# Performance work log

Measured on AMD Instinct MI355X. Metric: run time of the kernel, lower is better.

## Reference

```python
import jax, jax.numpy as jnp
import numpy as np

N = 8192      # nodes
DIN = 128     # in_channels
DH = 64       # hidden_channels (dim_out, num_heads=1)
DOUT = 32     # out_channels
RATIO = 0.5
K_KEEP = int(np.ceil(RATIO * N))  # SAGPooling keep count (single graph)
LN_EPS = 1e-5


def _linear_params(k, fan_in, fan_out):
    kw, kb = jax.random.split(k)
    W = jax.random.normal(kw, (fan_in, fan_out), dtype=jnp.float32) / jnp.sqrt(jnp.float32(fan_in))
    b = jax.random.normal(kb, (fan_out,), dtype=jnp.float32) * 0.01
    return W, b


def setup_inputs() -> dict:
    key = jax.random.key(0)
    ks = jax.random.split(key, 8)
    x = jax.random.normal(ks[0], (N, DIN), dtype=jnp.float32)
    batch = jnp.zeros((N,), dtype=jnp.int64)  # single graph
    Wq, bq = _linear_params(ks[1], DIN, DH)
    Wk, bk = _linear_params(ks[2], DIN, DH)
    Wv, bv = _linear_params(ks[3], DIN, DH)
    gcn_W, gcn_b = _linear_params(ks[4], DH, DH)       # GCNConv weight/bias
    score_W, score_b = _linear_params(ks[5], DH, 1)    # SAGPooling score GCNConv
    ln_g = jnp.ones((DH,), dtype=jnp.float32)
    ln_b = jnp.zeros((DH,), dtype=jnp.float32)
    head_W, head_b = _linear_params(ks[6], DH, DOUT)
    return dict(x=x, batch=batch, Wq=Wq, bq=bq, Wk=Wk, bk=bk, Wv=Wv, bv=bv,
                gcn_W=gcn_W, gcn_b=gcn_b, score_W=score_W, score_b=score_b,
                ln_g=ln_g, ln_b=ln_b, head_W=head_W, head_b=head_b)


def _forward(x, Wq, bq, Wk, bk, Wv, bv, gcn_W, gcn_b, score_W, score_b,
             ln_g, ln_b, head_W, head_b):
    # --- self-attention over all nodes (num_heads = 1) ---
    Q = x @ Wq + bq                                        # [N, DH]
    K = x @ Wk + bk
    V = x @ Wv + bv
    attn = jax.nn.softmax(Q @ K.T / jnp.sqrt(jnp.float32(DH)), axis=-1)  # [N, N]
    h = attn @ V                                           # [N, DH]

    # --- edge construction: threshold attention, ensure self-loops ---
    # (attn > 0.5).nonzero() -> edge set; empty -> self-loop fallback; then
    # add_self_loops. Dense equivalent: A = max(mask, I).
    eye = jnp.eye(N, dtype=x.dtype)
    A = jnp.maximum((attn > 0.5).astype(x.dtype), eye)     # [N, N], diag = 1

    # symmetric GCN normalization  D^{-1/2} A D^{-1/2}
    dinv = jax.lax.rsqrt(A.sum(axis=1))                    # [N]
    An = dinv[:, None] * A * dinv[None, :]                 # [N, N]

    # --- GCNConv layer ---
    g = An @ (h @ gcn_W) + gcn_b                           # [N, DH]

    # --- SAGPooling: GCNConv scorer -> tanh -> global top-k (single graph) ---
    score = jnp.tanh((An @ (g @ score_W) + score_b).squeeze(-1))  # [N]
    top_scores, perm = jax.lax.top_k(score, K_KEEP)        # sorted desc, like PyG topk
    xp = g[perm] * top_scores[:, None]                     # [K, DH], multiplier = 1

    # --- LayerNorm + ReLU (dropout is identity in eval) ---
    mu = xp.mean(axis=-1, keepdims=True)
    var = xp.var(axis=-1, keepdims=True)
    xp = (xp - mu) * jax.lax.rsqrt(var + LN_EPS) * ln_g + ln_b
    xp = jax.nn.relu(xp)

    # --- prediction head ---
    return xp @ head_W + head_b                            # [K, DOUT]


def reference(x, batch, Wq, bq, Wk, bk, Wv, bv, gcn_W, gcn_b,
              score_W, score_b, ln_g, ln_b, head_W, head_b):
    del batch  # single graph; grouping has no effect on the math
    return _forward(x, Wq, bq, Wk, bk, Wv, bv, gcn_W, gcn_b,
                    score_W, score_b, ln_g, ln_b, head_W, head_b)
```

## Files before the change

kernel.cpp:

```cpp
#include <hip/hip_runtime.h>
#include <hip/hip_bf16.h>
#include <cstdio>

typedef __hip_bfloat16 bf16;
typedef __attribute__((ext_vector_type(8))) short v8s;
typedef __attribute__((ext_vector_type(4))) short v4s;
typedef __attribute__((ext_vector_type(4))) float v4f;
typedef __attribute__((ext_vector_type(4))) double v4d;

#define MFMA16(a, b, c) __builtin_amdgcn_mfma_f32_16x16x32_bf16((a), (b), (c), 0, 0, 0)

#define NN 8192
#define DIN 128
#define DH 64
#define DOUT 32
#define KKEEP 4096
#define SPLITS 8
#define SPATT 8

__device__ __forceinline__ float bf2f(bf16 v) { return __bfloat162float(v); }
__device__ __forceinline__ short f2bfs(float f) {
  __hip_bfloat16 h = __float2bfloat16(f);
  return *reinterpret_cast<short*>(&h);
}
__device__ __forceinline__ bf16 f2bf(float v) { return __float2bfloat16(v); }

__device__ __forceinline__ double exp_d(double s) {
  const double L2E    = 1.4426950408889634074;
  const double LN2_HI = 6.93147180369123816490e-01;
  const double LN2_LO = 1.90821492927058770002e-10;
  double t  = s * L2E;
  double kf = rint(t);
  double r  = fma(-kf, LN2_HI, s);
  r = fma(-kf, LN2_LO, r);
  double p = 1.0 / 362880.0;
  p = fma(p, r, 1.0 / 40320.0);
  p = fma(p, r, 1.0 / 5040.0);
  p = fma(p, r, 1.0 / 720.0);
  p = fma(p, r, 1.0 / 120.0);
  p = fma(p, r, 1.0 / 24.0);
  p = fma(p, r, 1.0 / 6.0);
  p = fma(p, r, 0.5);
  p = fma(p, r, 1.0);
  p = fma(p, r, 1.0);
  int k = (int)kf;
  long long bits = ((long long)(1023 + k)) << 52;
  double sc = __longlong_as_double(bits);
  return p * sc;
}

__global__ void k0_ucb(const float* __restrict__ gW, const float* __restrict__ sW,
                       const float* __restrict__ gb, double* __restrict__ u) {
  int c = threadIdx.x;
  double acc = 0.0, accb = 0.0;
  for (int d = 0; d < DH; ++d) {
    double swd = (double)sW[d];
    acc  = fma((double)gW[c * DH + d], swd, acc);
    accb = fma((double)gb[d], swd, accb);
  }
  u[c] = acc;
  if (c == 0) u[64] = accb;
}

__global__ __launch_bounds__(256) void k1_prep(
    const float* __restrict__ x, const float* __restrict__ Wq, const float* __restrict__ bq,
    const float* __restrict__ Wk, const float* __restrict__ bk, const float* __restrict__ Wv,
    const float* __restrict__ bv, const double* __restrict__ u,
    double* __restrict__ Qd, double* __restrict__ Kd, double* __restrict__ w,
    bf16* __restrict__ Qb, bf16* __restrict__ Kb, bf16* __restrict__ Vt) {
  __shared__ double xs[16][DIN];
  int t = threadIdx.x;
  int nb = blockIdx.x * 16;
  for (int idx = t; idx < 16 * DIN; idx += 256)
    xs[idx >> 7][idx & 127] = (double)x[(size_t)nb * DIN + idx];
  __syncthreads();
  int d = t & 63;
  int sub = t >> 6;
  double bqd = (double)bq[d];
  double bkd = (double)bk[d];
  double bvd = (double)bv[d];
  double ud = u[d];
  for (int pass = 0; pass < 4; ++pass) {
    int n = pass * 4 + sub;
    double aq = bqd, ak = bkd, av = bvd;
#pragma unroll 8
    for (int c = 0; c < DIN; ++c) {
      double xv = xs[n][c];
      aq = fma(xv, (double)Wq[c * DH + d], aq);
      ak = fma(xv, (double)Wk[c * DH + d], ak);
      av = fma(xv, (double)Wv[c * DH + d], av);
    }
    aq *= 0.125;
    int node = nb + n;
    Qd[(size_t)node * DH + d] = aq;
    Kd[(size_t)node * DH + d] = ak;
    Qb[(size_t)node * DH + d] = f2bf((float)aq);
    Kb[(size_t)node * DH + d] = f2bf((float)ak);
    Vt[(size_t)d * NN + node] = f2bf((float)av);
    double pw = av * ud;
#pragma unroll
    for (int off = 32; off; off >>= 1) pw += __shfl_xor(pw, off);
    if (d == 0) w[node] = pw;
  }
}

__global__ __launch_bounds__(256) void k2_scores(
    const double* __restrict__ Qd, const double* __restrict__ Kd, const double* __restrict__ w,
    double* __restrict__ Zp, double* __restrict__ Wp, double* __restrict__ Ep, int* __restrict__ Jp) {
  __shared__ __align__(16) double Kbuf[2][16][66];
  const int t = threadIdx.x;
  const int wv = t >> 6;
  const int l = t & 63;
  const int li = l & 15, lg = l >> 4;
  const int rb = (blockIdx.x & 127) * 64;
  const int sp = blockIdx.x >> 7;
  const int cbeg = sp * (NN / SPLITS);

  double qreg[16];
  const double* qrow = Qd + (size_t)(rb + 16 * wv + li) * DH + lg;
#pragma unroll
  for (int tt = 0; tt < 16; ++tt) qreg[tt] = qrow[4 * tt];

  {
    const double* src = Kd + (size_t)cbeg * DH;
    int r = t >> 4, c = (t & 15) * 4;
    *(double2*)&Kbuf[0][r][c]     = *(const double2*)&src[r * DH + c];
    *(double2*)&Kbuf[0][r][c + 2] = *(const double2*)&src[r * DH + c + 2];
  }
  __syncthreads();

  double Zt[4] = {0, 0, 0, 0}, Wt[4] = {0, 0, 0, 0}, Et[4] = {-1, -1, -1, -1};
  int Jt[4] = {0, 0, 0, 0};

  const int NT = (NN / SPLITS) / 16;
  for (int kt = 0; kt < NT; ++kt) {
    const int buf = kt & 1;
    if (kt + 1 < NT) {
      const double* src = Kd + (size_t)(cbeg + (kt + 1) * 16) * DH;
      int r = t >> 4, c = (t & 15) * 4;
      *(double2*)&Kbuf[buf ^ 1][r][c]     = *(const double2*)&src[r * DH + c];
      *(double2*)&Kbuf[buf ^ 1][r][c + 2] = *(const double2*)&src[r * DH + c + 2];
    }
    v4d acc = (v4d){0.0, 0.0, 0.0, 0.0};
#pragma unroll
    for (int tt = 0; tt < 16; ++tt) {
      double bfrag = Kbuf[buf][li][4 * tt + lg];
      acc = __builtin_amdgcn_mfma_f64_16x16x4f64(qreg[tt], bfrag, acc, 0, 0, 0);
    }
    const int col = cbeg + kt * 16 + li;
    const double wj = w[col];
#pragma unroll
    for (int v = 0; v < 4; ++v) {
      double e = exp_d(acc[v]);
      Zt[v] += e;
      Wt[v] = fma(e, wj, Wt[v]);
      if (e > Et[v]) { Et[v] = e; Jt[v] = col; }
    }
    __syncthreads();
  }

#pragma unroll
  for (int v = 0; v < 4; ++v) {
#pragma unroll
    for (int m = 1; m < 16; m <<= 1) {
      Zt[v] += __shfl_xor(Zt[v], m);
      Wt[v] += __shfl_xor(Wt[v], m);
      double e2 = __shfl_xor(Et[v], m);
      int j2 = __shfl_xor(Jt[v], m);
      if (e2 > Et[v] || (e2 == Et[v] && j2 < Jt[v])) { Et[v] = e2; Jt[v] = j2; }
    }
  }
  if (li == 0) {
#pragma unroll
    for (int v = 0; v < 4; ++v) {
      int row = rb + 16 * wv + lg + 4 * v;
      Zp[sp * NN + row] = Zt[v];
      Wp[sp * NN + row] = Wt[v];
      Ep[sp * NN + row] = Et[v];
      Jp[sp * NN + row] = Jt[v];
    }
  }
}

__global__ void k3_combine(const double* __restrict__ Zp, const double* __restrict__ Wp,
                           const double* __restrict__ Ep, const int* __restrict__ Jp,
                           double* __restrict__ tau, int* __restrict__ extra, int* __restrict__ jmA) {
  int i = blockIdx.x * 256 + threadIdx.x;
  double Z = 0, W = 0, E = -1;
  int J = 0;
  for (int sp = 0; sp < SPLITS; ++sp) {
    Z += Zp[sp * NN + i];
    W += Wp[sp * NN + i];
    double e = Ep[sp * NN + i];
    if (e > E || (e == E && Jp[sp * NN + i] < J)) { E = e; J = Jp[sp * NN + i]; }
  }
  tau[i] = W / Z;
  extra[i] = (E > 0.5 * Z) && (J != i);
  jmA[i] = J & (NN - 1);
}

__global__ __launch_bounds__(256) void k4_mfma(const bf16* __restrict__ Qb, const bf16* __restrict__ Kb,
                                               const bf16* __restrict__ Vt,
                                               float* __restrict__ hp, float* __restrict__ zp) {
  __shared__ __align__(16) short P[4][16 * 40];
  const int t = threadIdx.x;
  const int wv = t >> 6;
  const int l = t & 63, g = l >> 4, li = l & 15;
  const int qb = (blockIdx.x & 127) * 64 + wv * 16;
  const int sp = blockIdx.x >> 7;
  short* Pw = &P[wv][0];
  const v8s q0 = *(const v8s*)(Qb + (size_t)(qb + li) * DH + g * 8);
  const v8s q1 = *(const v8s*)(Qb + (size_t)(qb + li) * DH + 32 + g * 8);
  v4f hacc[4];
#pragma unroll
  for (int db = 0; db < 4; ++db) hacc[db] = (v4f){0.f, 0.f, 0.f, 0.f};
  float zl = 0.f;
  const int kbeg = sp * (NN / SPATT);
  for (int jb = kbeg; jb < kbeg + NN / SPATT; jb += 32) {
    const bf16* kp = Kb + (size_t)(jb + li) * DH + g * 8;
    v8s ka0 = *(const v8s*)(kp);
    v8s ka1 = *(const v8s*)(kp + 32);
    v8s kb0 = *(const v8s*)(kp + 16 * DH);
    v8s kb1 = *(const v8s*)(kp + 16 * DH + 32);
    v4f c0 = (v4f){0.f, 0.f, 0.f, 0.f}, c1 = (v4f){0.f, 0.f, 0.f, 0.f};
    c0 = MFMA16(ka0, q0, c0);
    c0 = MFMA16(ka1, q1, c0);
    c1 = MFMA16(kb0, q0, c1);
    c1 = MFMA16(kb1, q1, c1);
    v4s p0, p1;
#pragma unroll
    for (int r = 0; r < 4; ++r) {
      short b0 = f2bfs(__expf(c0[r]));
      short b1 = f2bfs(__expf(c1[r]));
      p0[r] = b0;
      p1[r] = b1;
      zl += bf2f(*reinterpret_cast<bf16*>(&b0));
      zl += bf2f(*reinterpret_cast<bf16*>(&b1));
    }
    *(v4s*)&Pw[li * 40 + g * 4] = p0;
    *(v4s*)&Pw[li * 40 + 16 + g * 4] = p1;
    __syncthreads();
    v8s pf = *(const v8s*)&Pw[li * 40 + g * 8];
#pragma unroll
    for (int db = 0; db < 4; ++db) {
      const v8s vb = *(const v8s*)(Vt + (size_t)(db * 16 + li) * NN + jb + g * 8);
      hacc[db] = MFMA16(pf, vb, hacc[db]);
    }
    __syncthreads();
  }
  zl += __shfl_xor(zl, 16);
  zl += __shfl_xor(zl, 32);
  if (g == 0) zp[sp * NN + qb + li] = zl;
#pragma unroll
  for (int r = 0; r < 4; ++r) {
    int row = qb + g * 4 + r;
#pragma unroll
    for (int db = 0; db < 4; ++db)
      hp[((size_t)sp * NN + row) * DH + db * 16 + li] = hacc[db][r];
  }
}

__global__ __launch_bounds__(256) void k4_comb(const float* __restrict__ hp, const float* __restrict__ zp,
                                               float* __restrict__ h) {
  int i = blockIdx.x * 256 + threadIdx.x;
  int row = i >> 6;
  float Z = 0.f, H = 0.f;
#pragma unroll
  for (int sp = 0; sp < SPATT; ++sp) {
    Z += zp[sp * NN + row];
    H += hp[(size_t)sp * NN * DH + i];
  }
  h[i] = H / Z;
}

__global__ void k5_t(const double* __restrict__ tau, const int* __restrict__ extra,
                     const int* __restrict__ jmA, const double* __restrict__ u, double* __restrict__ tarr) {
  int i = blockIdx.x * 256 + threadIdx.x;
  int ex = extra[i];
  double di = ex ? 0.70710678118654752440 : 1.0;
  double acc = di * tau[i];
  if (ex) {
    int j = jmA[i] & (NN - 1);
    double dj = extra[j] ? 0.70710678118654752440 : 1.0;
    acc = fma(dj, tau[j], acc);
  }
  tarr[i] = fma(di, acc, u[64]);
}

__global__ void k6_pre(const double* __restrict__ tarr, const int* __restrict__ extra,
                       const int* __restrict__ jmA, const float* __restrict__ score_b,
                       double* __restrict__ pre, float* __restrict__ sc32, int* __restrict__ cnt) {
  int i = blockIdx.x * 256 + threadIdx.x;
  int ex = extra[i];
  double di = ex ? 0.70710678118654752440 : 1.0;
  double acc = di * tarr[i];
  if (ex) {
    int j = jmA[i] & (NN - 1);
    double dj = extra[j] ? 0.70710678118654752440 : 1.0;
    acc = fma(dj, tarr[j], acc);
  }
  double p = fma(di, acc, (double)score_b[0]);
  pre[i] = p;
  sc32[i] = (float)tanh(p);
  cnt[i] = 0;
}

__global__ void k7_rank(const double* __restrict__ pre, int* __restrict__ cnt) {
  int i = (blockIdx.x & 31) * 256 + threadIdx.x;
  int j0 = (blockIdx.x >> 5) * 512;
  double si = pre[i];
  int c = 0;
#pragma unroll 4
  for (int j = j0; j < j0 + 512; j += 2) {
    double2 pj = *(const double2*)(pre + j);
    c += (pj.x > si || (pj.x == si && j < i));
    c += (pj.y > si || (pj.y == si && (j + 1) < i));
  }
  atomicAdd(&cnt[i], c);
}

__global__ void k8_sel(const int* __restrict__ cnt, int* __restrict__ sel) {
  int i = blockIdx.x * 256 + threadIdx.x;
  unsigned r = (unsigned)cnt[i];
  if (r < KKEEP) sel[r] = i;
}

__global__ __launch_bounds__(256) void k9_M(const float* __restrict__ h, const float* __restrict__ gW,
                                            float* __restrict__ M) {
  int t = threadIdx.x;
  int n = blockIdx.x * 4 + (t >> 6);
  int d = t & 63;
  const float* hpn = h + (size_t)n * DH;
  float acc = 0.f;
#pragma unroll 8
  for (int c = 0; c < DH; ++c) acc = fmaf(hpn[c], gW[c * DH + d], acc);
  M[(size_t)n * DH + d] = acc;
}

__global__ void k10_g(const float* __restrict__ M, const int* __restrict__ extra,
                      const int* __restrict__ jmA, const float* __restrict__ gb, float* __restrict__ gbuf) {
  int i = blockIdx.x * 256 + threadIdx.x;
  int n = i >> 6, d = i & 63;
  int ex = extra[n];
  float di = ex ? 0.70710678f : 1.0f;
  float acc = di * M[i];
  if (ex) {
    int j = jmA[n] & (NN - 1);
    acc = fmaf(extra[j] ? 0.70710678f : 1.0f, M[j * DH + d], acc);
  }
  gbuf[i] = fmaf(di, acc, gb[d]);
}

__global__ __launch_bounds__(256) void k11_head(const float* __restrict__ gbuf, const float* __restrict__ sc32,
                                                const int* __restrict__ sel, const float* __restrict__ lg,
                                                const float* __restrict__ lb, const float* __restrict__ hW,
                                                const float* __restrict__ hb, float* __restrict__ out) {
  __shared__ float xs[4][DH];
  int t = threadIdx.x;
  int wv = t >> 6, d = t & 63;
  int p = blockIdx.x * 4 + wv;
  int i = sel[p] & (NN - 1);
  float v = gbuf[i * DH + d] * sc32[i];
  float s1 = v;
#pragma unroll
  for (int off = 32; off; off >>= 1) s1 += __shfl_xor(s1, off);
  float mu = s1 * (1.0f / 64.0f);
  float dv = v - mu;
  float s2 = dv * dv;
#pragma unroll
  for (int off = 32; off; off >>= 1) s2 += __shfl_xor(s2, off);
  float var = s2 * (1.0f / 64.0f);
  float xn = dv * rsqrtf(var + 1e-5f) * lg[d] + lb[d];
  xs[wv][d] = fmaxf(xn, 0.0f);
  __syncthreads();
  if (t < 128) {
    int r = t >> 5, o = t & 31;
    float acc = hb[o];
#pragma unroll 8
    for (int c = 0; c < DH; ++c) acc = fmaf(xs[r][c], hW[c * DOUT + o], acc);
    out[(size_t)(blockIdx.x * 4 + r) * DOUT + o] = acc;
  }
}

#define MB 1048576ull
constexpr size_t OFF_QD   = 0 * MB;
constexpr size_t OFF_KD   = 4 * MB;
constexpr size_t OFF_H    = 14 * MB;
constexpr size_t OFF_M    = 16 * MB;
constexpr size_t OFF_G    = 18 * MB;
constexpr size_t OFF_ZP   = 20 * MB;
constexpr size_t OFF_WP   = 21 * MB;
constexpr size_t OFF_EP   = 22 * MB;
constexpr size_t OFF_JP   = 23 * MB;
constexpr size_t OFF_W    = 24 * MB;
constexpr size_t OFF_U    = 25 * MB;
constexpr size_t OFF_TAU  = 26 * MB;
constexpr size_t OFF_EX   = 27 * MB;
constexpr size_t OFF_JM   = 28 * MB;
constexpr size_t OFF_T    = 29 * MB;
constexpr size_t OFF_PRE  = 30 * MB;
constexpr size_t OFF_SC   = 31 * MB;
constexpr size_t OFF_CNT  = 32 * MB;
constexpr size_t OFF_SEL  = 33 * MB;
constexpr size_t OFF_HP   = 34 * MB;
constexpr size_t OFF_ZATT = 50 * MB;
constexpr size_t OFF_QB   = 51 * MB;
constexpr size_t OFF_KB   = 52 * MB;
constexpr size_t OFF_VT   = 53 * MB;
constexpr size_t WS_NEEDED = 54 * MB;

extern "C" void kernel_launch(void* const* d_in, const int* in_sizes, int n_in,
                              void* d_out, int out_size, void* d_ws, size_t ws_size,
                              hipStream_t stream) {
  if (n_in < 16 || ws_size < WS_NEEDED || out_size != KKEEP * DOUT) {
    fprintf(stderr, "[sag] GUARD ws=%zu need=%zu n_in=%d out=%d\n", ws_size, WS_NEEDED, n_in, out_size);
    return;
  }
  const float* x   = (const float*)d_in[0];
  const float* Wq  = (const float*)d_in[2];
  const float* bq  = (const float*)d_in[3];
  const float* Wk  = (const float*)d_in[4];
  const float* bk  = (const float*)d_in[5];
  const float* Wv  = (const float*)d_in[6];
  const float* bv  = (const float*)d_in[7];
  const float* gW  = (const float*)d_in[8];
  const float* gb  = (const float*)d_in[9];
  const float* sW  = (const float*)d_in[10];
  const float* sb  = (const float*)d_in[11];
  const float* lg  = (const float*)d_in[12];
  const float* lb  = (const float*)d_in[13];
  const float* hW  = (const float*)d_in[14];
  const float* hb  = (const float*)d_in[15];
  float* out = (float*)d_out;

  char* ws = (char*)d_ws;
  double* Qd  = (double*)(ws + OFF_QD);
  double* Kd  = (double*)(ws + OFF_KD);
  bf16*   Qb  = (bf16*)(ws + OFF_QB);
  bf16*   Kb  = (bf16*)(ws + OFF_KB);
  bf16*   Vt  = (bf16*)(ws + OFF_VT);
  float*  h   = (float*)(ws + OFF_H);
  float*  M   = (float*)(ws + OFF_M);
  float*  g   = (float*)(ws + OFF_G);
  double* Zp  = (double*)(ws + OFF_ZP);
  double* Wp  = (double*)(ws + OFF_WP);
  double* Ep  = (double*)(ws + OFF_EP);
  int*    Jp  = (int*)(ws + OFF_JP);
  double* w   = (double*)(ws + OFF_W);
  double* u   = (double*)(ws + OFF_U);
  double* tau = (double*)(ws + OFF_TAU);
  int*    ex  = (int*)(ws + OFF_EX);
  int*    jm  = (int*)(ws + OFF_JM);
  double* tarr= (double*)(ws + OFF_T);
  double* pre = (double*)(ws + OFF_PRE);
  float*  sc32= (float*)(ws + OFF_SC);
  int*    cnt = (int*)(ws + OFF_CNT);
  int*    sel = (int*)(ws + OFF_SEL);
  float*  hp  = (float*)(ws + OFF_HP);
  float*  zatt= (float*)(ws + OFF_ZATT);

  hipLaunchKernelGGL(k0_ucb, dim3(1), dim3(64), 0, stream, gW, sW, gb, u);
  hipLaunchKernelGGL(k1_prep, dim3(512), dim3(256), 0, stream, x, Wq, bq, Wk, bk, Wv, bv, u,
                     Qd, Kd, w, Qb, Kb, Vt);
  hipLaunchKernelGGL(k2_scores, dim3(128 * SPLITS), dim3(256), 0, stream, Qd, Kd, w, Zp, Wp, Ep, Jp);
  hipLaunchKernelGGL(k3_combine, dim3(32), dim3(256), 0, stream, Zp, Wp, Ep, Jp, tau, ex, jm);
  hipLaunchKernelGGL(k4_mfma, dim3(128 * SPATT), dim3(256), 0, stream, Qb, Kb, Vt, hp, zatt);
  hipLaunchKernelGGL(k4_comb, dim3(2048), dim3(256), 0, stream, hp, zatt, h);
  hipLaunchKernelGGL(k9_M, dim3(2048), dim3(256), 0, stream, h, gW, M);
  hipLaunchKernelGGL(k5_t, dim3(32), dim3(256), 0, stream, tau, ex, jm, u, tarr);
  hipLaunchKernelGGL(k6_pre, dim3(32), dim3(256), 0, stream, tarr, ex, jm, sb, pre, sc32, cnt);
  hipLaunchKernelGGL(k7_rank, dim3(512), dim3(256), 0, stream, pre, cnt);
  hipLaunchKernelGGL(k8_sel, dim3(32), dim3(256), 0, stream, cnt, sel);
  hipLaunchKernelGGL(k10_g, dim3(2048), dim3(256), 0, stream, M, ex, jm, gb, g);
  hipLaunchKernelGGL(k11_head, dim3(1024), dim3(256), 0, stream, g, sc32, sel, lg, lb, hW, hb, out);
}
```

Measured before the change: 406.6 us.

## Fuse attention combine into GCN matmul, fuse gather into head, widen K tiles

Three changes. The split-attention combine is merged with the h@gcn_W product, so h is kept in shared memory and never written to global memory. The sparse GCN aggregation (k10) is folded into the head kernel, so it is computed only for the kept nodes and two launches disappear. The fp64 score kernel now stages 32 K rows per iteration instead of 16, which halves the barrier count at the cost of twice the LDS use.

```diff
diff --git a/kernel.cpp b/kernel.cpp
--- a/kernel.cpp
+++ b/kernel.cpp
@@ -107,7 +107,7 @@
 __global__ __launch_bounds__(256) void k2_scores(
     const double* __restrict__ Qd, const double* __restrict__ Kd, const double* __restrict__ w,
     double* __restrict__ Zp, double* __restrict__ Wp, double* __restrict__ Ep, int* __restrict__ Jp) {
-  __shared__ __align__(16) double Kbuf[2][16][66];
+  __shared__ __align__(16) double Kbuf[2][32][66];
   const int t = threadIdx.x;
   const int wv = t >> 6;
   const int l = t & 63;
@@ -123,38 +123,47 @@
 
   {
     const double* src = Kd + (size_t)cbeg * DH;
-    int r = t >> 4, c = (t & 15) * 4;
-    *(double2*)&Kbuf[0][r][c]     = *(const double2*)&src[r * DH + c];
-    *(double2*)&Kbuf[0][r][c + 2] = *(const double2*)&src[r * DH + c + 2];
+#pragma unroll
+    for (int k = 0; k < 4; ++k) {
+      int g = t + 256 * k;
+      int r = g >> 5, c2 = g & 31;
+      *(double2*)&Kbuf[0][r][c2 * 2] = *(const double2*)&src[r * DH + c2 * 2];
+    }
   }
   __syncthreads();
 
   double Zt[4] = {0, 0, 0, 0}, Wt[4] = {0, 0, 0, 0}, Et[4] = {-1, -1, -1, -1};
   int Jt[4] = {0, 0, 0, 0};
 
-  const int NT = (NN / SPLITS) / 16;
+  const int NT = (NN / SPLITS) / 32;
   for (int kt = 0; kt < NT; ++kt) {
     const int buf = kt & 1;
     if (kt + 1 < NT) {
-      const double* src = Kd + (size_t)(cbeg + (kt + 1) * 16) * DH;
-      int r = t >> 4, c = (t & 15) * 4;
-      *(double2*)&Kbuf[buf ^ 1][r][c]     = *(const double2*)&src[r * DH + c];
-      *(double2*)&Kbuf[buf ^ 1][r][c + 2] = *(const double2*)&src[r * DH + c + 2];
-    }
-    v4d acc = (v4d){0.0, 0.0, 0.0, 0.0};
-#pragma unroll
-    for (int tt = 0; tt < 16; ++tt) {
-      double bfrag = Kbuf[buf][li][4 * tt + lg];
-      acc = __builtin_amdgcn_mfma_f64_16x16x4f64(qreg[tt], bfrag, acc, 0, 0, 0);
-    }
-    const int col = cbeg + kt * 16 + li;
-    const double wj = w[col];
-#pragma unroll
-    for (int v = 0; v < 4; ++v) {
-      double e = exp_d(acc[v]);
-      Zt[v] += e;
-      Wt[v] = fma(e, wj, Wt[v]);
-      if (e > Et[v]) { Et[v] = e; Jt[v] = col; }
+      const double* src = Kd + (size_t)(cbeg + (kt + 1) * 32) * DH;
+#pragma unroll
+      for (int k = 0; k < 4; ++k) {
+        int g = t + 256 * k;
+        int r = g >> 5, c2 = g & 31;
+        *(double2*)&Kbuf[buf ^ 1][r][c2 * 2] = *(const double2*)&src[r * DH + c2 * 2];
+      }
+    }
+#pragma unroll
+    for (int hf = 0; hf < 2; ++hf) {
+      v4d acc = (v4d){0.0, 0.0, 0.0, 0.0};
+#pragma unroll
+      for (int tt = 0; tt < 16; ++tt) {
+        double bfrag = Kbuf[buf][li + 16 * hf][4 * tt + lg];
+        acc = __builtin_amdgcn_mfma_f64_16x16x4f64(qreg[tt], bfrag, acc, 0, 0, 0);
+      }
+      const int col = cbeg + kt * 32 + 16 * hf + li;
+      const double wj = w[col];
+#pragma unroll
+      for (int v = 0; v < 4; ++v) {
+        double e = exp_d(acc[v]);
+        Zt[v] += e;
+        Wt[v] = fma(e, wj, Wt[v]);
+        if (e > Et[v]) { Et[v] = e; Jt[v] = col; }
+      }
     }
     __syncthreads();
   }
@@ -260,17 +269,24 @@
   }
 }
 
-__global__ __launch_bounds__(256) void k4_comb(const float* __restrict__ hp, const float* __restrict__ zp,
-                                               float* __restrict__ h) {
-  int i = blockIdx.x * 256 + threadIdx.x;
-  int row = i >> 6;
+__global__ __launch_bounds__(256) void k9_hM(const float* __restrict__ hp, const float* __restrict__ zp,
+                                             const float* __restrict__ gW, float* __restrict__ M) {
+  __shared__ float xs[4][DH];
+  int t = threadIdx.x;
+  int sub = t >> 6, d = t & 63;
+  int n = blockIdx.x * 4 + sub;
   float Z = 0.f, H = 0.f;
 #pragma unroll
   for (int sp = 0; sp < SPATT; ++sp) {
-    Z += zp[sp * NN + row];
-    H += hp[(size_t)sp * NN * DH + i];
-  }
-  h[i] = H / Z;
+    Z += zp[sp * NN + n];
+    H += hp[((size_t)sp * NN + n) * DH + d];
+  }
+  xs[sub][d] = H / Z;
+  __syncthreads();
+  float acc = 0.f;
+#pragma unroll 8
+  for (int c = 0; c < DH; ++c) acc = fmaf(xs[sub][c], gW[c * DH + d], acc);
+  M[(size_t)n * DH + d] = acc;
 }
 
 __global__ void k5_t(const double* __restrict__ tau, const int* __restrict__ extra,
@@ -325,42 +341,26 @@
   if (r < KKEEP) sel[r] = i;
 }
 
-__global__ __launch_bounds__(256) void k9_M(const float* __restrict__ h, const float* __restrict__ gW,
-                                            float* __restrict__ M) {
-  int t = threadIdx.x;
-  int n = blockIdx.x * 4 + (t >> 6);
-  int d = t & 63;
-  const float* hpn = h + (size_t)n * DH;
-  float acc = 0.f;
-#pragma unroll 8
-  for (int c = 0; c < DH; ++c) acc = fmaf(hpn[c], gW[c * DH + d], acc);
-  M[(size_t)n * DH + d] = acc;
-}
-
-__global__ void k10_g(const float* __restrict__ M, const int* __restrict__ extra,
-                      const int* __restrict__ jmA, const float* __restrict__ gb, float* __restrict__ gbuf) {
-  int i = blockIdx.x * 256 + threadIdx.x;
-  int n = i >> 6, d = i & 63;
-  int ex = extra[n];
-  float di = ex ? 0.70710678f : 1.0f;
-  float acc = di * M[i];
-  if (ex) {
-    int j = jmA[n] & (NN - 1);
-    acc = fmaf(extra[j] ? 0.70710678f : 1.0f, M[j * DH + d], acc);
-  }
-  gbuf[i] = fmaf(di, acc, gb[d]);
-}
-
-__global__ __launch_bounds__(256) void k11_head(const float* __restrict__ gbuf, const float* __restrict__ sc32,
-                                                const int* __restrict__ sel, const float* __restrict__ lg,
-                                                const float* __restrict__ lb, const float* __restrict__ hW,
-                                                const float* __restrict__ hb, float* __restrict__ out) {
+__global__ __launch_bounds__(256) void k11_head(const float* __restrict__ M, const int* __restrict__ extra,
+                                                const int* __restrict__ jmA, const float* __restrict__ gb,
+                                                const float* __restrict__ sc32, const int* __restrict__ sel,
+                                                const float* __restrict__ lg, const float* __restrict__ lb,
+                                                const float* __restrict__ hW, const float* __restrict__ hb,
+                                                float* __restrict__ out) {
   __shared__ float xs[4][DH];
   int t = threadIdx.x;
   int wv = t >> 6, d = t & 63;
   int p = blockIdx.x * 4 + wv;
   int i = sel[p] & (NN - 1);
-  float v = gbuf[i * DH + d] * sc32[i];
+  int ex = extra[i];
+  float di = ex ? 0.70710678f : 1.0f;
+  float acc0 = di * M[(size_t)i * DH + d];
+  if (ex) {
+    int j = jmA[i] & (NN - 1);
+    acc0 = fmaf(extra[j] ? 0.70710678f : 1.0f, M[(size_t)j * DH + d], acc0);
+  }
+  float gval = fmaf(di, acc0, gb[d]);
+  float v = gval * sc32[i];
   float s1 = v;
 #pragma unroll
   for (int off = 32; off; off >>= 1) s1 += __shfl_xor(s1, off);
@@ -385,9 +385,7 @@
 #define MB 1048576ull
 constexpr size_t OFF_QD   = 0 * MB;
 constexpr size_t OFF_KD   = 4 * MB;
-constexpr size_t OFF_H    = 14 * MB;
 constexpr size_t OFF_M    = 16 * MB;
-constexpr size_t OFF_G    = 18 * MB;
 constexpr size_t OFF_ZP   = 20 * MB;
 constexpr size_t OFF_WP   = 21 * MB;
 constexpr size_t OFF_EP   = 22 * MB;
@@ -439,9 +437,7 @@
   bf16*   Qb  = (bf16*)(ws + OFF_QB);
   bf16*   Kb  = (bf16*)(ws + OFF_KB);
   bf16*   Vt  = (bf16*)(ws + OFF_VT);
-  float*  h   = (float*)(ws + OFF_H);
   float*  M   = (float*)(ws + OFF_M);
-  float*  g   = (float*)(ws + OFF_G);
   double* Zp  = (double*)(ws + OFF_ZP);
   double* Wp  = (double*)(ws + OFF_WP);
   double* Ep  = (double*)(ws + OFF_EP);
@@ -465,12 +461,11 @@
   hipLaunchKernelGGL(k2_scores, dim3(128 * SPLITS), dim3(256), 0, stream, Qd, Kd, w, Zp, Wp, Ep, Jp);
   hipLaunchKernelGGL(k3_combine, dim3(32), dim3(256), 0, stream, Zp, Wp, Ep, Jp, tau, ex, jm);
   hipLaunchKernelGGL(k4_mfma, dim3(128 * SPATT), dim3(256), 0, stream, Qb, Kb, Vt, hp, zatt);
-  hipLaunchKernelGGL(k4_comb, dim3(2048), dim3(256), 0, stream, hp, zatt, h);
-  hipLaunchKernelGGL(k9_M, dim3(2048), dim3(256), 0, stream, h, gW, M);
+  hipLaunchKernelGGL(k9_hM, dim3(2048), dim3(256), 0, stream, hp, zatt, gW, M);
   hipLaunchKernelGGL(k5_t, dim3(32), dim3(256), 0, stream, tau, ex, jm, u, tarr);
   hipLaunchKernelGGL(k6_pre, dim3(32), dim3(256), 0, stream, tarr, ex, jm, sb, pre, sc32, cnt);
   hipLaunchKernelGGL(k7_rank, dim3(512), dim3(256), 0, stream, pre, cnt);
   hipLaunchKernelGGL(k8_sel, dim3(32), dim3(256), 0, stream, cnt, sel);
-  hipLaunchKernelGGL(k10_g, dim3(2048), dim3(256), 0, stream, M, ex, jm, gb, g);
-  hipLaunchKernelGGL(k11_head, dim3(1024), dim3(256), 0, stream, g, sc32, sel, lg, lb, hW, hb, out);
-}
+  hipLaunchKernelGGL(k11_head, dim3(1024), dim3(256), 0, stream, M, ex, jm, gb, sc32, sel,
+                     lg, lb, hW, hb, out);
+}
```

New measurement: 407.5 us. No clear change (+0.2%).
